# Performance work log

Measured on AMD Instinct MI355X. Metric: run time of the kernel, lower is better.

## Reference

```python
import jax, jax.numpy as jnp
import numpy as np
import math

B, N, HID, NH = 128, 512, 512, 8
DH = HID // NH  # d_heads = 64


def setup_inputs() -> dict:
    key = jax.random.key(0)
    ks = jax.random.split(key, 8)
    s = 0.05  # keep logits in a sane range
    h = jax.random.normal(ks[0], (B, N, HID), dtype=jnp.float32)
    lengths = jax.random.randint(ks[1], (B,), 1, N + 1, dtype=jnp.int32)
    w_q = jax.random.normal(ks[2], (HID, HID), dtype=jnp.float32) * s
    w_k = jax.random.normal(ks[3], (HID, HID), dtype=jnp.float32) * s
    w_v = jax.random.normal(ks[4], (HID, HID), dtype=jnp.float32) * s
    w_o = jax.random.normal(ks[5], (HID, HID), dtype=jnp.float32) * s
    w_seed_w = jax.random.normal(ks[6], (HID, 1), dtype=jnp.float32) * s  # Linear(1, k*hidden), k=1
    w_seed_b = jax.random.normal(ks[7], (HID,), dtype=jnp.float32) * s
    seed_vec = jnp.ones((1,), dtype=jnp.float32)
    return {"h": h, "lengths": lengths, "w_q": w_q, "w_k": w_k, "w_v": w_v,
            "w_o": w_o, "w_seed_w": w_seed_w, "w_seed_b": w_seed_b, "seed_vec": seed_vec}


def reference(h, lengths, w_q, w_k, w_v, w_o, w_seed_w, w_seed_b, seed_vec):
    # PMA with k=1 seed query. norm_features=False.
    # query = w_seed(seed_vec), same for every graph in the batch.
    query = w_seed_w @ seed_vec + w_seed_b            # [HID]
    q = (w_q @ query).reshape(NH, DH)                 # [NH, DH] (Linear: x @ W.T == W @ x for vector)
    # NOTE: original code computes w_k(v) but never uses it in attention; output
    # depends only on q and v (e = q * v summed over d_heads). We skip the dead compute.
    v = (h @ w_v.T).reshape(B, N, NH, DH)             # [B, N, NH, DH]
    # logits: e[b,h,n] = <q[h], v[b,n,h]> / sqrt(DH)
    e = jnp.einsum("hd,bnhd->bhn", q, v) / math.sqrt(DH)
    valid = jnp.arange(N)[None, :] < lengths[:, None]  # [B, N] ragged mask
    e = jnp.where(valid[:, None, :], e, -jnp.inf)
    alpha = jax.nn.softmax(e, axis=-1)                # [B, NH, N]; padded cols -> 0
    out_h = jnp.einsum("bhn,bnhd->bhd", alpha, v)     # [B, NH, DH]
    out = out_h.reshape(B, HID) @ w_o.T               # [B*k, HID], packed (k=1)
    alpha_out = alpha[..., None]                      # [B, NH, N, 1] matching torch permute
    return out, alpha_out
```

## Files before the change

### kernel.cpp

```cpp
#include <hip/hip_runtime.h>
#include <math.h>

constexpr int B = 128, N = 512, HID = 512, NH = 8, DH = 64;

__global__ __launch_bounds__(64) void k1_qk(
    const float* __restrict__ w_q, const float* __restrict__ w_v,
    const float* __restrict__ w_sw, const float* __restrict__ w_sb,
    const float* __restrict__ seed, float* __restrict__ qk)
{
    __shared__ __align__(16) float query_s[HID];
    __shared__ float q_s[DH];
    const int t  = threadIdx.x;
    const int h  = blockIdx.x >> 3;
    const int jc = blockIdx.x & 7;
    const float sv = seed[0];
    #pragma unroll
    for (int k = 0; k < 8; ++k) {
        const int j = t * 8 + k;
        query_s[j] = w_sw[j] * sv + w_sb[j];
    }
    __syncthreads();
    {
        const float* row = w_q + (size_t)(h * DH + t) * HID;
        float acc = 0.f;
        for (int j = 0; j < HID; j += 4) {
            const float4 wv = *(const float4*)(row + j);
            acc += wv.x * query_s[j]     + wv.y * query_s[j + 1]
                 + wv.z * query_s[j + 2] + wv.w * query_s[j + 3];
        }
        q_s[t] = acc;
    }
    __syncthreads();
    {
        const int j = jc * 64 + t;
        float acc = 0.f;
        for (int d = 0; d < DH; ++d)
            acc += q_s[d] * w_v[(size_t)(h * DH + d) * HID + j];
        qk[h * HID + j] = acc * 0.125f;
    }
}

__global__ __launch_bounds__(256) void k2_e(
    const float* __restrict__ hbuf, const int* __restrict__ lengths,
    const float* __restrict__ qk, float* __restrict__ e_ws)
{
    __shared__ __align__(16) float qk_s[NH * HID];
    const int t = threadIdx.x;
    const int b = blockIdx.x >> 2;
    const int c = blockIdx.x & 3;
    for (int i = t * 4; i < NH * HID; i += 256 * 4)
        *(float4*)&qk_s[i] = *(const float4*)&qk[i];
    __syncthreads();

    const int r    = t >> 1;
    const int half = t & 1;
    const int n    = c * 128 + r;
    const int len  = lengths[b];
    if (n >= len) return;

    const float* row = hbuf + (size_t)(b * N + n) * HID + half * 4;
    float acc[NH];
    #pragma unroll
    for (int hh = 0; hh < NH; ++hh) acc[hh] = 0.f;

    for (int q8 = 0; q8 < HID; q8 += 8) {
        const float4 hv = *(const float4*)(row + q8);
        const int j = q8 + half * 4;
        #pragma unroll
        for (int hh = 0; hh < NH; ++hh) {
            const float4 qv = *(const float4*)&qk_s[hh * HID + j];
            acc[hh] += hv.x * qv.x + hv.y * qv.y + hv.z * qv.z + hv.w * qv.w;
        }
    }
    #pragma unroll
    for (int hh = 0; hh < NH; ++hh)
        acc[hh] += __shfl_xor(acc[hh], 1, 64);
    if (half == 0) {
        #pragma unroll
        for (int hh = 0; hh < NH; ++hh)
            e_ws[(size_t)(b * NH + hh) * N + n] = acc[hh];
    }
}

__global__ __launch_bounds__(256) void k2b_softmax(
    const float* __restrict__ e_ws, const int* __restrict__ lengths,
    float* __restrict__ alpha)
{
    const int b    = blockIdx.x;
    const int lane = threadIdx.x & 63;
    const int w    = threadIdx.x >> 6;
    const int len  = lengths[b];
    for (int hh = w; hh < NH; hh += 4) {
        const float* e = e_ws + (size_t)(b * NH + hh) * N;
        float ev[8];
        float m = -3.0e38f;
        #pragma unroll
        for (int it = 0; it < 8; ++it) {
            const int n = it * 64 + lane;
            ev[it] = (n < len) ? e[n] : -3.0e38f;
            m = fmaxf(m, ev[it]);
        }
        #pragma unroll
        for (int off = 32; off; off >>= 1)
            m = fmaxf(m, __shfl_xor(m, off, 64));
        float s = 0.f;
        #pragma unroll
        for (int it = 0; it < 8; ++it) {
            ev[it] = __expf(ev[it] - m);
            s += ev[it];
        }
        #pragma unroll
        for (int off = 32; off; off >>= 1)
            s += __shfl_xor(s, off, 64);
        const float inv = 1.f / s;
        float* ao = alpha + (size_t)(b * NH + hh) * N;
        #pragma unroll
        for (int it = 0; it < 8; ++it) {
            const int n = it * 64 + lane;
            ao[n] = (n < len) ? ev[it] * inv : 0.f;
        }
    }
}

__global__ __launch_bounds__(256) void k3_ctx(
    const float* __restrict__ hbuf, const int* __restrict__ lengths,
    const float* __restrict__ alpha, float* __restrict__ ctxp)
{
    __shared__ __align__(16) float al_s[128][8];
    const int t  = threadIdx.x;
    const int b  = blockIdx.x >> 2;
    const int c  = blockIdx.x & 3;
    const int n0 = c * 128;
    const int len = lengths[b];
    for (int i = t; i < 128 * 8; i += 256) {
        const int hh = i >> 7, nl = i & 127;
        al_s[nl][hh] = alpha[(size_t)(b * NH + hh) * N + n0 + nl];
    }
    __syncthreads();

    const int nend = min(len - n0, 128);
    float2 acc[NH];
    #pragma unroll
    for (int hh = 0; hh < NH; ++hh) { acc[hh].x = 0.f; acc[hh].y = 0.f; }

    const float* hb = hbuf + (size_t)(b * N + n0) * HID + t * 2;
    for (int ln = 0; ln < nend; ++ln) {
        const float2 hv = *(const float2*)(hb + (size_t)ln * HID);
        const float4 a0 = *(const float4*)&al_s[ln][0];
        const float4 a1 = *(const float4*)&al_s[ln][4];
        acc[0].x += a0.x * hv.x; acc[0].y += a0.x * hv.y;
        acc[1].x += a0.y * hv.x; acc[1].y += a0.y * hv.y;
        acc[2].x += a0.z * hv.x; acc[2].y += a0.z * hv.y;
        acc[3].x += a0.w * hv.x; acc[3].y += a0.w * hv.y;
        acc[4].x += a1.x * hv.x; acc[4].y += a1.x * hv.y;
        acc[5].x += a1.y * hv.x; acc[5].y += a1.y * hv.y;
        acc[6].x += a1.z * hv.x; acc[6].y += a1.z * hv.y;
        acc[7].x += a1.w * hv.x; acc[7].y += a1.w * hv.y;
    }
    #pragma unroll
    for (int hh = 0; hh < NH; ++hh)
        *(float2*)&ctxp[(size_t)((b * 4 + c) * NH + hh) * HID + t * 2] = acc[hh];
}

__global__ __launch_bounds__(256) void k4_out(
    const float* __restrict__ ctxp, const float* __restrict__ w_v,
    const float* __restrict__ w_o, float* __restrict__ out)
{
    __shared__ __align__(16) float ctx_s[NH * HID];
    __shared__ __align__(16) float oh_s[HID];
    const int t = threadIdx.x;
    const int b = blockIdx.x;
    const float* p0 = ctxp + (size_t)(b * 4) * NH * HID;
    for (int i = t; i < NH * HID; i += 256)
        ctx_s[i] = p0[i] + p0[NH * HID + i] + p0[2 * NH * HID + i] + p0[3 * NH * HID + i];
    __syncthreads();
    #pragma unroll
    for (int rep = 0; rep < 2; ++rep) {
        const int p  = rep * 256 + t;
        const int hh = p >> 6;
        const float* wrow = w_v + (size_t)p * HID;
        float acc = 0.f;
        for (int j = 0; j < HID; j += 4) {
            const float4 wv = *(const float4*)(wrow + j);
            const float4 cv = *(const float4*)&ctx_s[hh * HID + j];
            acc += wv.x * cv.x + wv.y * cv.y + wv.z * cv.z + wv.w * cv.w;
        }
        oh_s[p] = acc;
    }
    __syncthreads();
    #pragma unroll
    for (int rep = 0; rep < 2; ++rep) {
        const int i = rep * 256 + t;
        const float* wrow = w_o + (size_t)i * HID;
        float acc = 0.f;
        for (int j = 0; j < HID; j += 4) {
            const float4 wv = *(const float4*)(wrow + j);
            const float4 ov = *(const float4*)&oh_s[j];
            acc += wv.x * ov.x + wv.y * ov.y + wv.z * ov.z + wv.w * ov.w;
        }
        out[(size_t)b * HID + i] = acc;
    }
}

extern "C" void kernel_launch(void* const* d_in, const int* in_sizes, int n_in,
                              void* d_out, int out_size, void* d_ws, size_t ws_size,
                              hipStream_t stream) {
    const float* h     = (const float*)d_in[0];
    const int*   lens  = (const int*)  d_in[1];
    const float* w_q   = (const float*)d_in[2];
    const float* w_v   = (const float*)d_in[4];
    const float* w_o   = (const float*)d_in[5];
    const float* w_sw  = (const float*)d_in[6];
    const float* w_sb  = (const float*)d_in[7];
    const float* seed  = (const float*)d_in[8];

    float* out   = (float*)d_out;
    float* alpha = out + (size_t)B * HID;

    float* ws   = (float*)d_ws;
    float* qk   = ws;
    float* e_ws = qk + NH * HID;
    float* ctxp = e_ws + (size_t)B * NH * N;

    hipLaunchKernelGGL(k1_qk,       dim3(64),    dim3(64),  0, stream,
                       w_q, w_v, w_sw, w_sb, seed, qk);
    hipLaunchKernelGGL(k2_e,        dim3(B * 4), dim3(256), 0, stream,
                       h, lens, qk, e_ws);
    hipLaunchKernelGGL(k2b_softmax, dim3(B),     dim3(256), 0, stream,
                       e_ws, lens, alpha);
    hipLaunchKernelGGL(k3_ctx,      dim3(B * 4), dim3(256), 0, stream,
                       h, lens, alpha, ctxp);
    hipLaunchKernelGGL(k4_out,      dim3(B),     dim3(256), 0, stream,
                       ctxp, w_v, w_o, out);
}
```

Measured before the change: 310.2 us.

## Restructure logit and context kernels: split HID per wave, transpose alpha, double k3 grid

```diff
diff --git a/kernel.cpp b/kernel.cpp
--- a/kernel.cpp
+++ b/kernel.cpp
@@ -44,47 +44,54 @@
     const float* __restrict__ hbuf, const int* __restrict__ lengths,
     const float* __restrict__ qk, float* __restrict__ e_ws)
 {
-    __shared__ __align__(16) float qk_s[NH * HID];
-    const int t = threadIdx.x;
-    const int b = blockIdx.x >> 2;
-    const int c = blockIdx.x & 3;
-    for (int i = t * 4; i < NH * HID; i += 256 * 4)
-        *(float4*)&qk_s[i] = *(const float4*)&qk[i];
-    __syncthreads();
-
-    const int r    = t >> 1;
-    const int half = t & 1;
-    const int n    = c * 128 + r;
+    __shared__ float part[2][2][64][9];
+    const int t    = threadIdx.x;
+    const int lane = t & 63;
+    const int wave = t >> 6;
+    const int b    = blockIdx.x >> 2;
+    const int c    = blockIdx.x & 3;
+    const int g    = __builtin_amdgcn_readfirstlane(wave >> 1);
+    const int hb   = __builtin_amdgcn_readfirstlane(wave & 1);
+    const int n    = c * 128 + g * 64 + lane;
     const int len  = lengths[b];
-    if (n >= len) return;
-
-    const float* row = hbuf + (size_t)(b * N + n) * HID + half * 4;
+
     float acc[NH];
     #pragma unroll
     for (int hh = 0; hh < NH; ++hh) acc[hh] = 0.f;
 
-    for (int q8 = 0; q8 < HID; q8 += 8) {
-        const float4 hv = *(const float4*)(row + q8);
-        const int j = q8 + half * 4;
-        #pragma unroll
-        for (int hh = 0; hh < NH; ++hh) {
-            const float4 qv = *(const float4*)&qk_s[hh * HID + j];
-            acc[hh] += hv.x * qv.x + hv.y * qv.y + hv.z * qv.z + hv.w * qv.w;
+    if (n < len) {
+        const float* row = hbuf + (size_t)(b * N + n) * HID + hb * 256;
+        const float* qkb = qk + hb * 256;
+        #pragma unroll 4
+        for (int q = 0; q < 256; q += 8) {
+            const float4 h0 = *(const float4*)(row + q);
+            const float4 h1 = *(const float4*)(row + q + 4);
+            #pragma unroll
+            for (int hh = 0; hh < NH; ++hh) {
+                const float* qp = qkb + hh * HID + q;
+                acc[hh] += h0.x * qp[0] + h0.y * qp[1] + h0.z * qp[2] + h0.w * qp[3]
+                         + h1.x * qp[4] + h1.y * qp[5] + h1.z * qp[6] + h1.w * qp[7];
+            }
         }
     }
     #pragma unroll
     for (int hh = 0; hh < NH; ++hh)
-        acc[hh] += __shfl_xor(acc[hh], 1, 64);
-    if (half == 0) {
-        #pragma unroll
-        for (int hh = 0; hh < NH; ++hh)
-            e_ws[(size_t)(b * NH + hh) * N + n] = acc[hh];
+        part[g][hb][lane][hh] = acc[hh];
+    __syncthreads();
+
+    #pragma unroll
+    for (int v = t; v < 2 * 64 * NH; v += 256) {
+        const int gg = v >> 9, r = (v >> 3) & 63, hh = v & 7;
+        const int n2 = c * 128 + gg * 64 + r;
+        if (n2 < len)
+            e_ws[(size_t)(b * NH + hh) * N + n2] =
+                part[gg][0][r][hh] + part[gg][1][r][hh];
     }
 }
 
 __global__ __launch_bounds__(256) void k2b_softmax(
     const float* __restrict__ e_ws, const int* __restrict__ lengths,
-    float* __restrict__ alpha)
+    float* __restrict__ alpha, float* __restrict__ al_t)
 {
     const int b    = blockIdx.x;
     const int lane = threadIdx.x & 63;
@@ -114,52 +121,50 @@
             s += __shfl_xor(s, off, 64);
         const float inv = 1.f / s;
         float* ao = alpha + (size_t)(b * NH + hh) * N;
+        float* at = al_t + (size_t)b * N * NH + hh;
         #pragma unroll
         for (int it = 0; it < 8; ++it) {
-            const int n = it * 64 + lane;
-            ao[n] = (n < len) ? ev[it] * inv : 0.f;
+            const int n   = it * 64 + lane;
+            const float v = (n < len) ? ev[it] * inv : 0.f;
+            ao[n]         = v;
+            at[n * NH]    = v;
         }
     }
 }
 
 __global__ __launch_bounds__(256) void k3_ctx(
     const float* __restrict__ hbuf, const int* __restrict__ lengths,
-    const float* __restrict__ alpha, float* __restrict__ ctxp)
-{
-    __shared__ __align__(16) float al_s[128][8];
-    const int t  = threadIdx.x;
-    const int b  = blockIdx.x >> 2;
-    const int c  = blockIdx.x & 3;
-    const int n0 = c * 128;
+    const float* __restrict__ al_t, float* __restrict__ ctxp)
+{
+    const int t   = threadIdx.x;
+    const int b   = blockIdx.x >> 3;
+    const int c   = blockIdx.x & 7;
+    const int n0  = c * 64;
     const int len = lengths[b];
-    for (int i = t; i < 128 * 8; i += 256) {
-        const int hh = i >> 7, nl = i & 127;
-        al_s[nl][hh] = alpha[(size_t)(b * NH + hh) * N + n0 + nl];
-    }
-    __syncthreads();
-
-    const int nend = min(len - n0, 128);
+    const int nend = min(len - n0, 64);
+
     float2 acc[NH];
     #pragma unroll
     for (int hh = 0; hh < NH; ++hh) { acc[hh].x = 0.f; acc[hh].y = 0.f; }
 
     const float* hb = hbuf + (size_t)(b * N + n0) * HID + t * 2;
+    const float* ap = al_t + (size_t)(b * N + n0) * NH;
+    #pragma unroll 2
     for (int ln = 0; ln < nend; ++ln) {
         const float2 hv = *(const float2*)(hb + (size_t)ln * HID);
-        const float4 a0 = *(const float4*)&al_s[ln][0];
-        const float4 a1 = *(const float4*)&al_s[ln][4];
-        acc[0].x += a0.x * hv.x; acc[0].y += a0.x * hv.y;
-        acc[1].x += a0.y * hv.x; acc[1].y += a0.y * hv.y;
-        acc[2].x += a0.z * hv.x; acc[2].y += a0.z * hv.y;
-        acc[3].x += a0.w * hv.x; acc[3].y += a0.w * hv.y;
-        acc[4].x += a1.x * hv.x; acc[4].y += a1.x * hv.y;
-        acc[5].x += a1.y * hv.x; acc[5].y += a1.y * hv.y;
-        acc[6].x += a1.z * hv.x; acc[6].y += a1.z * hv.y;
-        acc[7].x += a1.w * hv.x; acc[7].y += a1.w * hv.y;
+        const float* a = ap + ln * NH;
+        acc[0].x += a[0] * hv.x; acc[0].y += a[0] * hv.y;
+        acc[1].x += a[1] * hv.x; acc[1].y += a[1] * hv.y;
+        acc[2].x += a[2] * hv.x; acc[2].y += a[2] * hv.y;
+        acc[3].x += a[3] * hv.x; acc[3].y += a[3] * hv.y;
+        acc[4].x += a[4] * hv.x; acc[4].y += a[4] * hv.y;
+        acc[5].x += a[5] * hv.x; acc[5].y += a[5] * hv.y;
+        acc[6].x += a[6] * hv.x; acc[6].y += a[6] * hv.y;
+        acc[7].x += a[7] * hv.x; acc[7].y += a[7] * hv.y;
     }
     #pragma unroll
     for (int hh = 0; hh < NH; ++hh)
-        *(float2*)&ctxp[(size_t)((b * 4 + c) * NH + hh) * HID + t * 2] = acc[hh];
+        *(float2*)&ctxp[(size_t)((b * 8 + c) * NH + hh) * HID + t * 2] = acc[hh];
 }
 
 __global__ __launch_bounds__(256) void k4_out(
@@ -170,9 +175,13 @@
     __shared__ __align__(16) float oh_s[HID];
     const int t = threadIdx.x;
     const int b = blockIdx.x;
-    const float* p0 = ctxp + (size_t)(b * 4) * NH * HID;
-    for (int i = t; i < NH * HID; i += 256)
-        ctx_s[i] = p0[i] + p0[NH * HID + i] + p0[2 * NH * HID + i] + p0[3 * NH * HID + i];
+    const float* p0 = ctxp + (size_t)(b * 8) * NH * HID;
+    for (int i = t; i < NH * HID; i += 256) {
+        float s = 0.f;
+        #pragma unroll
+        for (int cc = 0; cc < 8; ++cc) s += p0[cc * NH * HID + i];
+        ctx_s[i] = s;
+    }
     __syncthreads();
     #pragma unroll
     for (int rep = 0; rep < 2; ++rep) {
@@ -220,16 +229,17 @@
     float* ws   = (float*)d_ws;
     float* qk   = ws;
     float* e_ws = qk + NH * HID;
-    float* ctxp = e_ws + (size_t)B * NH * N;
+    float* al_t = e_ws + (size_t)B * NH * N;
+    float* ctxp = al_t + (size_t)B * N * NH;
 
     hipLaunchKernelGGL(k1_qk,       dim3(64),    dim3(64),  0, stream,
                        w_q, w_v, w_sw, w_sb, seed, qk);
     hipLaunchKernelGGL(k2_e,        dim3(B * 4), dim3(256), 0, stream,
                        h, lens, qk, e_ws);
     hipLaunchKernelGGL(k2b_softmax, dim3(B),     dim3(256), 0, stream,
-                       e_ws, lens, alpha);
-    hipLaunchKernelGGL(k3_ctx,      dim3(B * 4), dim3(256), 0, stream,
-                       h, lens, alpha, ctxp);
+                       e_ws, lens, alpha, al_t);
+    hipLaunchKernelGGL(k3_ctx,      dim3(B * 8), dim3(256), 0, stream,
+                       h, lens, al_t, ctxp);
     hipLaunchKernelGGL(k4_out,      dim3(B),     dim3(256), 0, stream,
                        ctxp, w_v, w_o, out);
 }
```

Measured after the change: 305.7 us. About the same (-1.4%).

## Fuse logits, softmax, context and output projection into one per-batch kernel

Applied to the files above, without the earlier changes.

```diff
diff --git a/kernel.cpp b/kernel.cpp
--- a/kernel.cpp
+++ b/kernel.cpp
@@ -40,64 +40,55 @@
     }
 }
 
-__global__ __launch_bounds__(256) void k2_e(
+__global__ __launch_bounds__(512) void ka_fused(
     const float* __restrict__ hbuf, const int* __restrict__ lengths,
-    const float* __restrict__ qk, float* __restrict__ e_ws)
+    const float* __restrict__ qk, const float* __restrict__ w_v,
+    const float* __restrict__ w_o, float* __restrict__ out,
+    float* __restrict__ alpha)
 {
-    __shared__ __align__(16) float qk_s[NH * HID];
-    const int t = threadIdx.x;
-    const int b = blockIdx.x >> 2;
-    const int c = blockIdx.x & 3;
-    for (int i = t * 4; i < NH * HID; i += 256 * 4)
-        *(float4*)&qk_s[i] = *(const float4*)&qk[i];
+    __shared__ __align__(16) float e_s[N][12];
+    __shared__ __align__(16) float part_s[4 * NH * HID];
+    __shared__ __align__(16) float ctx_s[NH * HID];
+    __shared__ __align__(16) float oh_s[HID];
+    const int t   = threadIdx.x;
+    const int b   = blockIdx.x;
+    const int len = lengths[b];
+
+    {
+        const int wbase = __builtin_amdgcn_readfirstlane(t) & ~63;
+        if (wbase < len) {
+            const int n  = t;
+            const int nn = min(n, len - 1);
+            const float* row = hbuf + ((size_t)b * N + nn) * HID;
+            float acc[NH];
+            #pragma unroll
+            for (int hh = 0; hh < NH; ++hh) acc[hh] = 0.f;
+            #pragma unroll 2
+            for (int j = 0; j < HID; j += 4) {
+                const float4 hv = *(const float4*)(row + j);
+                #pragma unroll
+                for (int hh = 0; hh < NH; ++hh) {
+                    const float* qp = qk + hh * HID + j;
+                    acc[hh] += hv.x * qp[0] + hv.y * qp[1]
+                             + hv.z * qp[2] + hv.w * qp[3];
+                }
+            }
+            #pragma unroll
+            for (int hh = 0; hh < NH; ++hh)
+                e_s[n][hh] = (n < len) ? acc[hh] : -3.0e38f;
+        }
+    }
     __syncthreads();
 
-    const int r    = t >> 1;
-    const int half = t & 1;
-    const int n    = c * 128 + r;
-    const int len  = lengths[b];
-    if (n >= len) return;
-
-    const float* row = hbuf + (size_t)(b * N + n) * HID + half * 4;
-    float acc[NH];
-    #pragma unroll
-    for (int hh = 0; hh < NH; ++hh) acc[hh] = 0.f;
-
-    for (int q8 = 0; q8 < HID; q8 += 8) {
-        const float4 hv = *(const float4*)(row + q8);
-        const int j = q8 + half * 4;
-        #pragma unroll
-        for (int hh = 0; hh < NH; ++hh) {
-            const float4 qv = *(const float4*)&qk_s[hh * HID + j];
-            acc[hh] += hv.x * qv.x + hv.y * qv.y + hv.z * qv.z + hv.w * qv.w;
-        }
-    }
-    #pragma unroll
-    for (int hh = 0; hh < NH; ++hh)
-        acc[hh] += __shfl_xor(acc[hh], 1, 64);
-    if (half == 0) {
-        #pragma unroll
-        for (int hh = 0; hh < NH; ++hh)
-            e_ws[(size_t)(b * NH + hh) * N + n] = acc[hh];
-    }
-}
-
-__global__ __launch_bounds__(256) void k2b_softmax(
-    const float* __restrict__ e_ws, const int* __restrict__ lengths,
-    float* __restrict__ alpha)
-{
-    const int b    = blockIdx.x;
-    const int lane = threadIdx.x & 63;
-    const int w    = threadIdx.x >> 6;
-    const int len  = lengths[b];
-    for (int hh = w; hh < NH; hh += 4) {
-        const float* e = e_ws + (size_t)(b * NH + hh) * N;
+    {
+        const int lane = t & 63;
+        const int w    = t >> 6;
         float ev[8];
         float m = -3.0e38f;
         #pragma unroll
         for (int it = 0; it < 8; ++it) {
             const int n = it * 64 + lane;
-            ev[it] = (n < len) ? e[n] : -3.0e38f;
+            ev[it] = (n < len) ? e_s[n][w] : -3.0e38f;
             m = fmaxf(m, ev[it]);
         }
         #pragma unroll
@@ -113,70 +104,50 @@
         for (int off = 32; off; off >>= 1)
             s += __shfl_xor(s, off, 64);
         const float inv = 1.f / s;
-        float* ao = alpha + (size_t)(b * NH + hh) * N;
+        float* ao = alpha + (size_t)(b * NH + w) * N;
         #pragma unroll
         for (int it = 0; it < 8; ++it) {
-            const int n = it * 64 + lane;
-            ao[n] = (n < len) ? ev[it] * inv : 0.f;
+            const int n   = it * 64 + lane;
+            const float v = (n < len) ? ev[it] * inv : 0.f;
+            ao[n]      = v;
+            e_s[n][w]  = v;
         }
-    }
-}
-
-__global__ __launch_bounds__(256) void k3_ctx(
-    const float* __restrict__ hbuf, const int* __restrict__ lengths,
-    const float* __restrict__ alpha, float* __restrict__ ctxp)
-{
-    __shared__ __align__(16) float al_s[128][8];
-    const int t  = threadIdx.x;
-    const int b  = blockIdx.x >> 2;
-    const int c  = blockIdx.x & 3;
-    const int n0 = c * 128;
-    const int len = lengths[b];
-    for (int i = t; i < 128 * 8; i += 256) {
-        const int hh = i >> 7, nl = i & 127;
-        al_s[nl][hh] = alpha[(size_t)(b * NH + hh) * N + n0 + nl];
     }
     __syncthreads();
 
-    const int nend = min(len - n0, 128);
-    float2 acc[NH];
-    #pragma unroll
-    for (int hh = 0; hh < NH; ++hh) { acc[hh].x = 0.f; acc[hh].y = 0.f; }
+    {
+        const int q  = t >> 7;
+        const int cq = t & 127;
+        float4 acc[NH];
+        #pragma unroll
+        for (int hh = 0; hh < NH; ++hh) { acc[hh].x = acc[hh].y = acc[hh].z = acc[hh].w = 0.f; }
+        const float* hb = hbuf + (size_t)b * N * HID + cq * 4;
+        for (int n = q; n < len; n += 4) {
+            const float4 hv = *(const float4*)(hb + (size_t)n * HID);
+            const float4 a0 = *(const float4*)&e_s[n][0];
+            const float4 a1 = *(const float4*)&e_s[n][4];
+            acc[0].x += a0.x * hv.x; acc[0].y += a0.x * hv.y; acc[0].z += a0.x * hv.z; acc[0].w += a0.x * hv.w;
+            acc[1].x += a0.y * hv.x; acc[1].y += a0.y * hv.y; acc[1].z += a0.y * hv.z; acc[1].w += a0.y * hv.w;
+            acc[2].x += a0.z * hv.x; acc[2].y += a0.z * hv.y; acc[2].z += a0.z * hv.z; acc[2].w += a0.z * hv.w;
+            acc[3].x += a0.w * hv.x; acc[3].y += a0.w * hv.y; acc[3].z += a0.w * hv.z; acc[3].w += a0.w * hv.w;
+            acc[4].x += a1.x * hv.x; acc[4].y += a1.x * hv.y; acc[4].z += a1.x * hv.z; acc[4].w += a1.x * hv.w;
+            acc[5].x += a1.y * hv.x; acc[5].y += a1.y * hv.y; acc[5].z += a1.y * hv.z; acc[5].w += a1.y * hv.w;
+            acc[6].x += a1.z * hv.x; acc[6].y += a1.z * hv.y; acc[6].z += a1.z * hv.z; acc[6].w += a1.z * hv.w;
+            acc[7].x += a1.w * hv.x; acc[7].y += a1.w * hv.y; acc[7].z += a1.w * hv.z; acc[7].w += a1.w * hv.w;
+        }
+        #pragma unroll
+        for (int hh = 0; hh < NH; ++hh)
+            *(float4*)&part_s[(q * NH + hh) * HID + cq * 4] = acc[hh];
+    }
+    __syncthreads();
 
-    const float* hb = hbuf + (size_t)(b * N + n0) * HID + t * 2;
-    for (int ln = 0; ln < nend; ++ln) {
-        const float2 hv = *(const float2*)(hb + (size_t)ln * HID);
-        const float4 a0 = *(const float4*)&al_s[ln][0];
-        const float4 a1 = *(const float4*)&al_s[ln][4];
-        acc[0].x += a0.x * hv.x; acc[0].y += a0.x * hv.y;
-        acc[1].x += a0.y * hv.x; acc[1].y += a0.y * hv.y;
-        acc[2].x += a0.z * hv.x; acc[2].y += a0.z * hv.y;
-        acc[3].x += a0.w * hv.x; acc[3].y += a0.w * hv.y;
-        acc[4].x += a1.x * hv.x; acc[4].y += a1.x * hv.y;
-        acc[5].x += a1.y * hv.x; acc[5].y += a1.y * hv.y;
-        acc[6].x += a1.z * hv.x; acc[6].y += a1.z * hv.y;
-        acc[7].x += a1.w * hv.x; acc[7].y += a1.w * hv.y;
-    }
-    #pragma unroll
-    for (int hh = 0; hh < NH; ++hh)
-        *(float2*)&ctxp[(size_t)((b * 4 + c) * NH + hh) * HID + t * 2] = acc[hh];
-}
+    for (int i = t; i < NH * HID; i += 512)
+        ctx_s[i] = part_s[i] + part_s[NH * HID + i]
+                 + part_s[2 * NH * HID + i] + part_s[3 * NH * HID + i];
+    __syncthreads();
 
-__global__ __launch_bounds__(256) void k4_out(
-    const float* __restrict__ ctxp, const float* __restrict__ w_v,
-    const float* __restrict__ w_o, float* __restrict__ out)
-{
-    __shared__ __align__(16) float ctx_s[NH * HID];
-    __shared__ __align__(16) float oh_s[HID];
-    const int t = threadIdx.x;
-    const int b = blockIdx.x;
-    const float* p0 = ctxp + (size_t)(b * 4) * NH * HID;
-    for (int i = t; i < NH * HID; i += 256)
-        ctx_s[i] = p0[i] + p0[NH * HID + i] + p0[2 * NH * HID + i] + p0[3 * NH * HID + i];
-    __syncthreads();
-    #pragma unroll
-    for (int rep = 0; rep < 2; ++rep) {
-        const int p  = rep * 256 + t;
+    {
+        const int p  = t;
         const int hh = p >> 6;
         const float* wrow = w_v + (size_t)p * HID;
         float acc = 0.f;
@@ -188,9 +159,9 @@
         oh_s[p] = acc;
     }
     __syncthreads();
-    #pragma unroll
-    for (int rep = 0; rep < 2; ++rep) {
-        const int i = rep * 256 + t;
+
+    {
+        const int i = t;
         const float* wrow = w_o + (size_t)i * HID;
         float acc = 0.f;
         for (int j = 0; j < HID; j += 4) {
@@ -217,19 +188,10 @@
     float* out   = (float*)d_out;
     float* alpha = out + (size_t)B * HID;
 
-    float* ws   = (float*)d_ws;
-    float* qk   = ws;
-    float* e_ws = qk + NH * HID;
-    float* ctxp = e_ws + (size_t)B * NH * N;
+    float* qk = (float*)d_ws;
 
-    hipLaunchKernelGGL(k1_qk,       dim3(64),    dim3(64),  0, stream,
+    hipLaunchKernelGGL(k1_qk,    dim3(64), dim3(64),  0, stream,
                        w_q, w_v, w_sw, w_sb, seed, qk);
-    hipLaunchKernelGGL(k2_e,        dim3(B * 4), dim3(256), 0, stream,
-                       h, lens, qk, e_ws);
-    hipLaunchKernelGGL(k2b_softmax, dim3(B),     dim3(256), 0, stream,
-                       e_ws, lens, alpha);
-    hipLaunchKernelGGL(k3_ctx,      dim3(B * 4), dim3(256), 0, stream,
-                       h, lens, alpha, ctxp);
-    hipLaunchKernelGGL(k4_out,      dim3(B),     dim3(256), 0, stream,
-                       ctxp, w_v, w_o, out);
+    hipLaunchKernelGGL(ka_fused, dim3(B),  dim3(512), 0, stream,
+                       h, lens, qk, w_v, w_o, out, alpha);
 }
```

New measurement: 326.9 us. 1.05x slower.
